# Optimization experiments

Measured on AMD Instinct MI355X. Metric: run time of the kernel, lower is better.

The kernel has to match this reference:

```python
import jax, jax.numpy as jnp
import numpy as np
import math

B, C, L = 16, 512, 1024

def setup_inputs() -> dict:
    key = jax.random.key(0)
    kq, kk, kv = jax.random.split(key, 3)
    q = jax.random.normal(kq, (B, C, L), dtype=jnp.float32)
    k = jax.random.normal(kk, (B, C, L), dtype=jnp.float32)
    v = jax.random.normal(kv, (B, C, L), dtype=jnp.float32)
    return {"q": q, "k": k, "v": v}

def reference(q, k, v):
    # q, k, v: (b, c, l)
    b, c, l = q.shape
    # score[b, i, j] = sum_c k[b, c, i] * q[b, c, j]  -> (b, l, l)
    score = jnp.einsum('bci,bcj->bij', k, q) / math.sqrt(l)
    # Faithful to torch nn.Softmax() with dim=None on a 3D tensor:
    # torch's _get_softmax_dim picks dim=1 for ndim not in (0,1,3); ndim==3 -> dim=0.
    score = jax.nn.softmax(score, axis=0)
    # out[b, c, j] = sum_i v[b, c, i] * score[b, i, j]  -> (b, c, l)
    out = jnp.einsum('bci,bij->bcj', v, score)
    return out
```

## Files before the change

kernel.cpp:

```cpp
#include <hip/hip_runtime.h>
#include <hip/hip_bf16.h>


#define LN 1024
#define CC 512
#define BN 16

typedef __attribute__((ext_vector_type(8))) short bf16x8;
typedef __attribute__((ext_vector_type(4))) float f32x4;

static __device__ __forceinline__ unsigned short f2bf(float x) {
  union { float f; unsigned u; } un; un.f = x;
  unsigned r = un.u + 0x7fffu + ((un.u >> 16) & 1u);
  return (unsigned short)(r >> 16);
}
static __device__ __forceinline__ float bf2f(unsigned short h) {
  union { unsigned u; float f; } un; un.u = ((unsigned)h) << 16; return un.f;
}

__global__ __launch_bounds__(256) void transpose_convert(
    const float* __restrict__ q, const float* __restrict__ k,
    unsigned short* __restrict__ qT, unsigned short* __restrict__ kT) {
  __shared__ float tile[32][33];
  const int b   = blockIdx.z >> 1;
  const int mat = blockIdx.z & 1;
  const float* src = mat ? k : q;
  unsigned short* dst = mat ? kT : qT;
  const int l0 = blockIdx.x * 32, c0 = blockIdx.y * 32;
  const int t = threadIdx.x;
  const int ll = t & 31, cbase = t >> 5;
  const float* sp = src + ((size_t)b * CC + c0) * LN + l0;
#pragma unroll
  for (int r = 0; r < 4; ++r) {
    int cc = cbase + r * 8;
    tile[cc][ll] = sp[(size_t)cc * LN + ll];
  }
  __syncthreads();
  const int co = t & 31, lbase = t >> 5;
  unsigned short* dp = dst + ((size_t)b * LN + l0) * CC + c0;
#pragma unroll
  for (int r = 0; r < 4; ++r) {
    int lo = lbase + r * 8;
    dp[(size_t)lo * CC + co] = f2bf(tile[co][lo]);
  }
}

template<int KD, int LDAv, int LDBv, int LDCv, bool OBF>
__global__ __launch_bounds__(256) void gemm_bt(
    const unsigned short* __restrict__ A, const unsigned short* __restrict__ B,
    void* __restrict__ Cv, float scale,
    size_t strideA, size_t strideB, size_t strideC) {
  __shared__ unsigned short As[128 * 40];
  __shared__ unsigned short Bs[128 * 40];
  const int bz = blockIdx.z;
  const unsigned short* Ab = A + (size_t)bz * strideA;
  const unsigned short* Bb = B + (size_t)bz * strideB;
  const int tm = blockIdx.y, tn = blockIdx.x;
  const int t = threadIdx.x, w = t >> 6, l = t & 63;
  const int wr = w >> 1, wc = w & 1;
  const int lr = l & 15, lk8 = (l >> 4) * 8;

  f32x4 acc[4][4];
#pragma unroll
  for (int m = 0; m < 4; ++m)
#pragma unroll
    for (int n = 0; n < 4; ++n) acc[m][n] = (f32x4){0.f, 0.f, 0.f, 0.f};

  auto gA = [&](int q, int c0) -> bf16x8 {
    return *(const bf16x8*)(Ab + (size_t)(tm * 128 + (q >> 2)) * LDAv + c0 + (q & 3) * 8);
  };
  auto gB = [&](int q, int c0) -> bf16x8 {
    return *(const bf16x8*)(Bb + (size_t)(tn * 128 + (q >> 2)) * LDBv + c0 + (q & 3) * 8);
  };

  bf16x8 ra0 = gA(t, 0), ra1 = gA(t + 256, 0);
  bf16x8 rb0 = gB(t, 0), rb1 = gB(t + 256, 0);

  const int NSTEP = KD / 32;
#pragma unroll 1
  for (int step = 0; step < NSTEP; ++step) {
    __syncthreads();
    *(bf16x8*)(&As[(t >> 2) * 40 + (t & 3) * 8]) = ra0;
    *(bf16x8*)(&As[((t + 256) >> 2) * 40 + (t & 3) * 8]) = ra1;
    *(bf16x8*)(&Bs[(t >> 2) * 40 + (t & 3) * 8]) = rb0;
    *(bf16x8*)(&Bs[((t + 256) >> 2) * 40 + (t & 3) * 8]) = rb1;
    if (step + 1 < NSTEP) {
      const int c0 = (step + 1) * 32;
      ra0 = gA(t, c0); ra1 = gA(t + 256, c0);
      rb0 = gB(t, c0); rb1 = gB(t + 256, c0);
    }
    __syncthreads();
    bf16x8 af[4], bfr[4];
#pragma unroll
    for (int m = 0; m < 4; ++m)
      af[m] = *(const bf16x8*)(&As[(wr * 64 + m * 16 + lr) * 40 + lk8]);
#pragma unroll
    for (int n = 0; n < 4; ++n)
      bfr[n] = *(const bf16x8*)(&Bs[(wc * 64 + n * 16 + lr) * 40 + lk8]);
#pragma unroll
    for (int m = 0; m < 4; ++m)
#pragma unroll
      for (int n = 0; n < 4; ++n)
        acc[m][n] = __builtin_amdgcn_mfma_f32_16x16x32_bf16(af[m], bfr[n], acc[m][n], 0, 0, 0);
  }

#pragma unroll
  for (int m = 0; m < 4; ++m)
#pragma unroll
    for (int n = 0; n < 4; ++n)
#pragma unroll
      for (int r = 0; r < 4; ++r) {
        const int row = tm * 128 + wr * 64 + m * 16 + (l >> 4) * 4 + r;
        const int col = tn * 128 + wc * 64 + n * 16 + lr;
        if (OBF) {
          ((unsigned short*)Cv)[bz * strideC + (size_t)row * LDCv + col] =
              f2bf(acc[m][n][r] * scale);
        } else {
          ((float*)Cv)[bz * strideC + (size_t)row * LDCv + col] = acc[m][n][r] * scale;
        }
      }
}

__global__ __launch_bounds__(256) void convert_v(
    const float* __restrict__ v, unsigned short* __restrict__ vB) {
  const size_t i8 = (size_t)blockIdx.x * 256 + threadIdx.x;
  const float4 a = *(const float4*)(v + i8 * 8);
  const float4 b = *(const float4*)(v + i8 * 8 + 4);
  bf16x8 o;
  o[0] = (short)f2bf(a.x); o[1] = (short)f2bf(a.y);
  o[2] = (short)f2bf(a.z); o[3] = (short)f2bf(a.w);
  o[4] = (short)f2bf(b.x); o[5] = (short)f2bf(b.y);
  o[6] = (short)f2bf(b.z); o[7] = (short)f2bf(b.w);
  *(bf16x8*)(vB + i8 * 8) = o;
}

__global__ __launch_bounds__(256) void softmax_b(unsigned short* __restrict__ SP) {
  const size_t off = ((size_t)blockIdx.x * 256 + threadIdx.x) * 8;
  bf16x8 s[BN];
#pragma unroll
  for (int b = 0; b < BN; ++b)
    s[b] = *(const bf16x8*)(SP + (size_t)b * (LN * LN) + off);
#pragma unroll
  for (int e = 0; e < 8; ++e) {
    float vv[BN];
#pragma unroll
    for (int b = 0; b < BN; ++b) vv[b] = bf2f((unsigned short)s[b][e]);
    float m = vv[0];
#pragma unroll
    for (int b = 1; b < BN; ++b) m = fmaxf(m, vv[b]);
    float t[BN], sum = 0.f;
#pragma unroll
    for (int b = 0; b < BN; ++b) { t[b] = __expf(vv[b] - m); sum += t[b]; }
    const float inv = 1.f / sum;
#pragma unroll
    for (int b = 0; b < BN; ++b) s[b][e] = (short)f2bf(t[b] * inv);
  }
#pragma unroll
  for (int b = 0; b < BN; ++b)
    *(bf16x8*)(SP + (size_t)b * (LN * LN) + off) = s[b];
}

extern "C" void kernel_launch(void* const* d_in, const int* in_sizes, int n_in,
                              void* d_out, int out_size, void* d_ws, size_t ws_size,
                              hipStream_t stream) {
  const float* q = (const float*)d_in[0];
  const float* k = (const float*)d_in[1];
  const float* v = (const float*)d_in[2];
  float* out = (float*)d_out;

  unsigned short* qT = (unsigned short*)d_ws;
  unsigned short* kT = qT + (size_t)BN * LN * CC;
  unsigned short* SP = kT + (size_t)BN * LN * CC;
  unsigned short* vB = qT;

  transpose_convert<<<dim3(LN / 32, CC / 32, BN * 2), 256, 0, stream>>>(q, k, qT, kT);
  gemm_bt<512, 512, 512, 1024, true><<<dim3(8, 8, BN), 256, 0, stream>>>(
      qT, kT, (void*)SP, 0.03125f,
      (size_t)LN * CC, (size_t)LN * CC, (size_t)LN * LN);
  convert_v<<<dim3((BN * CC * LN) / 8 / 256), 256, 0, stream>>>(v, vB);
  softmax_b<<<dim3((LN * LN) / 8 / 256), 256, 0, stream>>>(SP);
  gemm_bt<1024, 1024, 1024, 1024, false><<<dim3(8, 4, BN), 256, 0, stream>>>(
      vB, SP, (void*)out, 1.0f,
      (size_t)CC * LN, (size_t)LN * LN, (size_t)CC * LN);
}
```

Baseline: 104.0 us.

## Use direct global-to-LDS loads with double buffering and XOR swizzle in GEMM

Replaces the register-staged LDS fill in the GEMM with global_load_lds direct copies into a double-buffered shared-memory tile. The K step grows from 32 to 64, and an XOR swizzle on the 16-byte slots avoids bank conflicts in place of padding. The aim is to overlap the next tile's loads with MFMA work and to cut VGPR traffic and barriers per K element. In exchange it uses four times more LDS (64 KB per block), which may lower occupancy, and it relies on the per-wave layout of global_load_lds matching the swizzled indexing.

```diff
diff --git a/kernel.cpp b/kernel.cpp
--- a/kernel.cpp
+++ b/kernel.cpp
@@ -46,19 +46,19 @@
 }
 
 template<int KD, int LDAv, int LDBv, int LDCv, bool OBF>
-__global__ __launch_bounds__(256) void gemm_bt(
+__global__ __launch_bounds__(256) void gemm_glds(
     const unsigned short* __restrict__ A, const unsigned short* __restrict__ B,
     void* __restrict__ Cv, float scale,
     size_t strideA, size_t strideB, size_t strideC) {
-  __shared__ unsigned short As[128 * 40];
-  __shared__ unsigned short Bs[128 * 40];
+  __shared__ unsigned short As[2][128 * 64];
+  __shared__ unsigned short Bs[2][128 * 64];
   const int bz = blockIdx.z;
   const unsigned short* Ab = A + (size_t)bz * strideA;
   const unsigned short* Bb = B + (size_t)bz * strideB;
   const int tm = blockIdx.y, tn = blockIdx.x;
   const int t = threadIdx.x, w = t >> 6, l = t & 63;
   const int wr = w >> 1, wc = w & 1;
-  const int lr = l & 15, lk8 = (l >> 4) * 8;
+  const int lr = l & 15, lks = l >> 4;
 
   f32x4 acc[4][4];
 #pragma unroll
@@ -66,42 +66,65 @@
 #pragma unroll
     for (int n = 0; n < 4; ++n) acc[m][n] = (f32x4){0.f, 0.f, 0.f, 0.f};
 
-  auto gA = [&](int q, int c0) -> bf16x8 {
-    return *(const bf16x8*)(Ab + (size_t)(tm * 128 + (q >> 2)) * LDAv + c0 + (q & 3) * 8);
+  const int srow = t >> 3;
+  const int sslot = t & 7;
+  const int wvbase = (w * 8) * 64;
+
+  auto STAGE = [&](int buf, int step) {
+    const int c0 = step * 64;
+#pragma unroll
+    for (int qq = 0; qq < 4; ++qq) {
+      const int row = qq * 32 + srow;
+      const unsigned short* ga =
+          Ab + (size_t)(tm * 128 + row) * LDAv + c0 + ((sslot ^ (row & 7)) * 8);
+      __builtin_amdgcn_global_load_lds(
+          (const __attribute__((address_space(1))) void*)ga,
+          (__attribute__((address_space(3))) void*)&As[buf][qq * 32 * 64 + wvbase],
+          16, 0, 0);
+    }
+#pragma unroll
+    for (int qq = 0; qq < 4; ++qq) {
+      const int row = qq * 32 + srow;
+      const unsigned short* gb =
+          Bb + (size_t)(tn * 128 + row) * LDBv + c0 + ((sslot ^ (row & 7)) * 8);
+      __builtin_amdgcn_global_load_lds(
+          (const __attribute__((address_space(1))) void*)gb,
+          (__attribute__((address_space(3))) void*)&Bs[buf][qq * 32 * 64 + wvbase],
+          16, 0, 0);
+    }
   };
-  auto gB = [&](int q, int c0) -> bf16x8 {
-    return *(const bf16x8*)(Bb + (size_t)(tn * 128 + (q >> 2)) * LDBv + c0 + (q & 3) * 8);
-  };
-
-  bf16x8 ra0 = gA(t, 0), ra1 = gA(t + 256, 0);
-  bf16x8 rb0 = gB(t, 0), rb1 = gB(t + 256, 0);
-
-  const int NSTEP = KD / 32;
+
+  STAGE(0, 0);
+  __syncthreads();
+
+  const int NSTEP = KD / 64;
+  int cur = 0;
 #pragma unroll 1
   for (int step = 0; step < NSTEP; ++step) {
-    __syncthreads();
-    *(bf16x8*)(&As[(t >> 2) * 40 + (t & 3) * 8]) = ra0;
-    *(bf16x8*)(&As[((t + 256) >> 2) * 40 + (t & 3) * 8]) = ra1;
-    *(bf16x8*)(&Bs[(t >> 2) * 40 + (t & 3) * 8]) = rb0;
-    *(bf16x8*)(&Bs[((t + 256) >> 2) * 40 + (t & 3) * 8]) = rb1;
-    if (step + 1 < NSTEP) {
-      const int c0 = (step + 1) * 32;
-      ra0 = gA(t, c0); ra1 = gA(t + 256, c0);
-      rb0 = gB(t, c0); rb1 = gB(t + 256, c0);
+    if (step + 1 < NSTEP) STAGE(cur ^ 1, step + 1);
+#pragma unroll
+    for (int kk = 0; kk < 2; ++kk) {
+      bf16x8 af[4], bfr[4];
+#pragma unroll
+      for (int m = 0; m < 4; ++m) {
+        const int r = wr * 64 + m * 16 + lr;
+        const int slot = (kk * 4 + lks) ^ (r & 7);
+        af[m] = *(const bf16x8*)(&As[cur][r * 64 + slot * 8]);
+      }
+#pragma unroll
+      for (int n = 0; n < 4; ++n) {
+        const int r = wc * 64 + n * 16 + lr;
+        const int slot = (kk * 4 + lks) ^ (r & 7);
+        bfr[n] = *(const bf16x8*)(&Bs[cur][r * 64 + slot * 8]);
+      }
+#pragma unroll
+      for (int m = 0; m < 4; ++m)
+#pragma unroll
+        for (int n = 0; n < 4; ++n)
+          acc[m][n] = __builtin_amdgcn_mfma_f32_16x16x32_bf16(af[m], bfr[n], acc[m][n], 0, 0, 0);
     }
     __syncthreads();
-    bf16x8 af[4], bfr[4];
-#pragma unroll
-    for (int m = 0; m < 4; ++m)
-      af[m] = *(const bf16x8*)(&As[(wr * 64 + m * 16 + lr) * 40 + lk8]);
-#pragma unroll
-    for (int n = 0; n < 4; ++n)
-      bfr[n] = *(const bf16x8*)(&Bs[(wc * 64 + n * 16 + lr) * 40 + lk8]);
-#pragma unroll
-    for (int m = 0; m < 4; ++m)
-#pragma unroll
-      for (int n = 0; n < 4; ++n)
-        acc[m][n] = __builtin_amdgcn_mfma_f32_16x16x32_bf16(af[m], bfr[n], acc[m][n], 0, 0, 0);
+    cur ^= 1;
   }
 
 #pragma unroll
@@ -148,12 +171,12 @@
     float m = vv[0];
 #pragma unroll
     for (int b = 1; b < BN; ++b) m = fmaxf(m, vv[b]);
-    float t[BN], sum = 0.f;
-#pragma unroll
-    for (int b = 0; b < BN; ++b) { t[b] = __expf(vv[b] - m); sum += t[b]; }
+    float tt[BN], sum = 0.f;
+#pragma unroll
+    for (int b = 0; b < BN; ++b) { tt[b] = __expf(vv[b] - m); sum += tt[b]; }
     const float inv = 1.f / sum;
 #pragma unroll
-    for (int b = 0; b < BN; ++b) s[b][e] = (short)f2bf(t[b] * inv);
+    for (int b = 0; b < BN; ++b) s[b][e] = (short)f2bf(tt[b] * inv);
   }
 #pragma unroll
   for (int b = 0; b < BN; ++b)
@@ -174,12 +197,12 @@
   unsigned short* vB = qT;
 
   transpose_convert<<<dim3(LN / 32, CC / 32, BN * 2), 256, 0, stream>>>(q, k, qT, kT);
-  gemm_bt<512, 512, 512, 1024, true><<<dim3(8, 8, BN), 256, 0, stream>>>(
+  gemm_glds<512, 512, 512, 1024, true><<<dim3(8, 8, BN), 256, 0, stream>>>(
       qT, kT, (void*)SP, 0.03125f,
       (size_t)LN * CC, (size_t)LN * CC, (size_t)LN * LN);
   convert_v<<<dim3((BN * CC * LN) / 8 / 256), 256, 0, stream>>>(v, vB);
   softmax_b<<<dim3((LN * LN) / 8 / 256), 256, 0, stream>>>(SP);
-  gemm_bt<1024, 1024, 1024, 1024, false><<<dim3(8, 4, BN), 256, 0, stream>>>(
+  gemm_glds<1024, 1024, 1024, 1024, false><<<dim3(8, 4, BN), 256, 0, stream>>>(
       vB, SP, (void*)out, 1.0f,
       (size_t)CC * LN, (size_t)LN * LN, (size_t)CC * LN);
 }
```

Result: faster. 100.3 us (-3.5%).
